# Kernel tuning notes

Measured on AMD Instinct MI355X. Metric: run time of the kernel, lower is better.

## Reference

```python
import jax, jax.numpy as jnp
import numpy as np

DROPOUT_P = 0.5  # eval-mode: hidden scaled by (1 - p) each step


def setup_inputs() -> dict:
    key = jax.random.key(0)
    ks = jax.random.split(key, 4)
    S, B, F, H = 512, 256, 256, 1024
    x = jax.random.normal(ks[0], (S, B, F), dtype=jnp.float32)
    W_i2h = jax.random.normal(ks[1], (H, F), dtype=jnp.float32) * 0.001
    b_i2h = jnp.zeros((H,), dtype=jnp.float32)
    W_h2h = jax.random.normal(ks[2], (H, H), dtype=jnp.float32) * 0.001
    init_hidden = jax.random.normal(ks[3], (1, 1, H), dtype=jnp.float32)
    return {"x": x, "W_i2h": W_i2h, "b_i2h": b_i2h, "W_h2h": W_h2h,
            "init_hidden": init_hidden, "batch_size": B}


def reference(x, W_i2h, b_i2h, W_h2h, init_hidden, batch_size):
    # x: [S, B, F] time-major. Output: final hidden [1, B, H].
    S, B, F = x.shape
    H = W_h2h.shape[0]
    keep = 1.0 - DROPOUT_P
    # Precompute input projections for all timesteps (batched GEMM).
    xi = jnp.einsum('sbf,hf->sbh', x, W_i2h) + b_i2h  # [S, B, H]
    # init_hidden [1,1,H] expanded to [B,H]
    h0 = jnp.broadcast_to(init_hidden[0], (B, H))

    def step(h, xi_t):
        # hidden = tanh(i2h(x_t) + h2h(keep * hidden))
        h_new = jnp.tanh(xi_t + (keep * h) @ W_h2h.T)
        return h_new, None

    h_final, _ = jax.lax.scan(step, h0, xi)
    return h_final[None]  # [1, B, H] matching torch broadcast shape
```

## Files before the change

kernel.cpp:

```cpp
#include <hip/hip_runtime.h>
#include <hip/hip_bf16.h>

#define S_LEN 512
#define B_SZ  256
#define F_SZ  256
#define H_SZ  1024
#define BH    (B_SZ * H_SZ)
#define KEEP  0.5f

typedef float f32x4 __attribute__((ext_vector_type(4)));
typedef short s16x8 __attribute__((ext_vector_type(8)));
typedef int   i32x4 __attribute__((ext_vector_type(4)));

static __device__ __forceinline__ short f2bf(float f) {
    unsigned u = __builtin_bit_cast(unsigned, f);
    unsigned r = u + 0x7fffu + ((u >> 16) & 1u);
    return (short)(r >> 16);
}

static __device__ __forceinline__ s16x8 pack8(f32x4 lo, f32x4 hi, float s) {
    s16x8 r;
#pragma unroll
    for (int i = 0; i < 4; ++i) { r[i] = f2bf(lo[i] * s); r[i + 4] = f2bf(hi[i] * s); }
    return r;
}

static __device__ __forceinline__ s16x8 pack8_pk(f32x4 lo, f32x4 hi) {
    int w0, w1, w2, w3;
    asm("v_cvt_pk_bf16_f32 %0, %1, %2" : "=v"(w0) : "v"(lo[0]), "v"(lo[1]));
    asm("v_cvt_pk_bf16_f32 %0, %1, %2" : "=v"(w1) : "v"(lo[2]), "v"(lo[3]));
    asm("v_cvt_pk_bf16_f32 %0, %1, %2" : "=v"(w2) : "v"(hi[0]), "v"(hi[1]));
    asm("v_cvt_pk_bf16_f32 %0, %1, %2" : "=v"(w3) : "v"(hi[2]), "v"(hi[3]));
    i32x4 r = { w0, w1, w2, w3 };
    return __builtin_bit_cast(s16x8, r);
}

static __device__ __forceinline__ long pack4_pk(f32x4 a) {
    int lo, hi;
    asm("v_cvt_pk_bf16_f32 %0, %1, %2" : "=v"(lo) : "v"(a[0]), "v"(a[1]));
    asm("v_cvt_pk_bf16_f32 %0, %1, %2" : "=v"(hi) : "v"(a[2]), "v"(a[3]));
    return (long)(((unsigned long)(unsigned)hi << 32) | (unsigned)lo);
}

static __device__ __forceinline__ f32x4 unpack4(long v) {
    unsigned lo = (unsigned)v, hi = (unsigned)((unsigned long)v >> 32);
    f32x4 r;
    r[0] = __builtin_bit_cast(float, lo << 16);
    r[1] = __builtin_bit_cast(float, lo & 0xffff0000u);
    r[2] = __builtin_bit_cast(float, hi << 16);
    r[3] = __builtin_bit_cast(float, hi & 0xffff0000u);
    return r;
}

static __device__ __forceinline__ float fast_tanh(float v) {
    float e = __expf(2.0f * v);
    return (e - 1.0f) / (e + 1.0f);
}

#define SYS_LD(p)   __hip_atomic_load((p), __ATOMIC_RELAXED, __HIP_MEMORY_SCOPE_SYSTEM)
#define SYS_ST(p,v) __hip_atomic_store((p), (v), __ATOMIC_RELAXED, __HIP_MEMORY_SCOPE_SYSTEM)
#define AGT_LD(p)   __hip_atomic_load((p), __ATOMIC_RELAXED, __HIP_MEMORY_SCOPE_AGENT)

template<int PURE>
static __device__ __forceinline__ int rmw_flag(int* p, int v) {
    int r;
    if constexpr (PURE)
        asm volatile("global_atomic_add %0, %1, %2, off sc0\n\ts_waitcnt vmcnt(0)"
                     : "=v"(r) : "v"(p), "v"(v) : "memory");
    else
        asm volatile("global_atomic_add %0, %1, %2, off sc0 sc1\n\ts_waitcnt vmcnt(0)"
                     : "=v"(r) : "v"(p), "v"(v) : "memory");
    return r;
}

template<int PURE>
static __device__ __forceinline__ void sig_flag(int* p) {
    int one = 1;
    if constexpr (PURE)
        asm volatile("global_atomic_add %0, %1, off" :: "v"(p), "v"(one) : "memory");
    else
        asm volatile("global_atomic_add %0, %1, off sc1" :: "v"(p), "v"(one) : "memory");
}

template<int PURE>
static __device__ __forceinline__ void sth(short* p, short v) {
    int vi = v;
    if constexpr (PURE)
        asm volatile("global_store_short %0, %1, off" :: "v"(p), "v"(vi) : "memory");
    else
        asm volatile("global_store_short %0, %1, off sc0 sc1" :: "v"(p), "v"(vi) : "memory");
}

#define MFMA(A, B, C) __builtin_amdgcn_mfma_f32_16x16x32_bf16((A), (B), (C), 0, 0, 0)

template<int PURE, int XI>
static __device__ __forceinline__ void step_loop(
    const float* __restrict__ x, const float* __restrict__ h0,
    float* __restrict__ out, short* __restrict__ hbuf, int* __restrict__ flags,
    const char* __restrict__ xi_lane, char* h_lds,
    const s16x8 (&wh)[32], const s16x8 (&wif)[8], float bj,
    int g, int b0, int role, int j, int wIdx, int wave, int lane, int tid, int dmask)
{
    const int ln = lane & 15;
    const int lk = lane >> 4;
    const int arow = b0 + ln;
    const int crow = b0 + lk * 4;
    const int xr = (ln & 7) << 4;
    const int rbase = ln * 2048 + lk * 16;
    int* const inbox  = flags + role * 64;
    int* const fanout = flags + ((g * 16 + lane) * 64 + wIdx);

    long xv = 0;
    if constexpr (XI) xv = *(const long*)xi_lane;

#pragma unroll 1
    for (int s = 0; s < S_LEN; ++s) {
        f32x4 acc[4];
        acc[1] = f32x4{ 0.f, 0.f, 0.f, 0.f };
        acc[2] = f32x4{ 0.f, 0.f, 0.f, 0.f };
        acc[3] = f32x4{ 0.f, 0.f, 0.f, 0.f };

        if constexpr (!XI) {
            acc[0] = f32x4{ bj, bj, bj, bj };
            const float* xp = x + ((size_t)s * B_SZ + arow) * F_SZ + lk * 8;
#pragma unroll
            for (int kf = 0; kf < 8; ++kf) {
                s16x8 a = pack8(*(const f32x4*)(xp + kf * 32),
                                *(const f32x4*)(xp + kf * 32 + 4), 1.0f);
                acc[kf & 1] = MFMA(a, wif[kf], acc[kf & 1]);
            }
        }

        if (s > 0) {
            if (wave == 0) {
                int it = 0;
                for (;;) {
                    int v = rmw_flag<PURE>(inbox + lane, 0);
                    if (__all(v >= s)) break;
                    if (++it > (1 << 14)) break;
                    __builtin_amdgcn_s_sleep(1);
                }
            }
            __syncthreads();

            const char* slice = (const char*)(hbuf + (size_t)((s - 1) & dmask) * BH
                                              + (size_t)b0 * H_SZ);
            long o[16];
#pragma unroll
            for (int r = 0; r < 16; ++r) {
                const long* p = (const long*)(slice + r * 2048) + tid;
                o[r] = PURE ? AGT_LD(p) : SYS_LD(p);
            }
#pragma unroll
            for (int r = 0; r < 16; ++r)
                *(long*)(h_lds + ((r * 2048 + tid * 8) ^ ((r & 7) << 4))) = o[r];
            __syncthreads();
            if constexpr (XI) acc[0] = unpack4(xv);

#pragma unroll
            for (int ks = 0; ks < 32; ++ks) {
                s16x8 a = *(const s16x8*)(h_lds + ((rbase + ks * 64) ^ xr));
                acc[ks & 3] = MFMA(a, wh[ks], acc[ks & 3]);
            }
        } else {
            if constexpr (XI) acc[0] = unpack4(xv);
#pragma unroll
            for (int ks = 0; ks < 32; ++ks) {
                const float* p = h0 + ks * 32 + lk * 8;
                s16x8 a = pack8(*(const f32x4*)p, *(const f32x4*)(p + 4), KEEP);
                acc[ks & 3] = MFMA(a, wh[ks], acc[ks & 3]);
            }
        }

        f32x4 r4 = (acc[0] + acc[1]) + (acc[2] + acc[3]);

        if (s < S_LEN - 1) {
            short* op = hbuf + (size_t)(s & dmask) * BH;
#pragma unroll
            for (int r = 0; r < 4; ++r)
                sth<PURE>(op + (crow + r) * H_SZ + j, f2bf(KEEP * fast_tanh(r4[r])));
            asm volatile("s_waitcnt vmcnt(0)" ::: "memory");
            if (lane < 16) sig_flag<PURE>(fanout);
            if constexpr (XI)
                xv = *(const long*)(xi_lane + (size_t)(s + 1) * (256u * 4 * 64 * 8));
        } else {
#pragma unroll
            for (int r = 0; r < 4; ++r)
                out[(crow + r) * H_SZ + j] = fast_tanh(r4[r]);
        }
    }
}

__global__ __launch_bounds__(256, 1) void xi_gemm(
    const float* __restrict__ x, const float* __restrict__ Wi,
    const float* __restrict__ bias, char* __restrict__ xi)
{
    const int bid  = blockIdx.x;
    const int role = bid & 255;
    const int c    = bid >> 8;
    const int g    = role >> 4;
    const int t    = role & 15;
    const int tid  = threadIdx.x;
    const int wave = tid >> 6;
    const int lane = tid & 63;
    const int ln   = lane & 15;
    const int lk   = lane >> 4;

    const int b0    = g * 16;
    const int jtile = t * 64;

    s16x8 wia[4][8];
    float b4[4];
#pragma unroll
    for (int jt = 0; jt < 4; ++jt) {
        b4[jt] = bias[jtile + jt * 16 + ln];
#pragma unroll
        for (int kf = 0; kf < 8; ++kf) {
            const float* p = Wi + (size_t)(jtile + jt * 16 + ln) * F_SZ
                           + kf * 32 + lk * 8;
            wia[jt][kf] = pack8_pk(*(const f32x4*)p, *(const f32x4*)(p + 4));
        }
    }

#pragma unroll 1
    for (int i = 0; i < 16; ++i) {
        const int s = c * 64 + wave + 4 * i;
        const float* xp = x + ((size_t)s * B_SZ + b0 + ln) * F_SZ + lk * 8;
        s16x8 af[8];
#pragma unroll
        for (int kf = 0; kf < 8; ++kf)
            af[kf] = pack8_pk(*(const f32x4*)(xp + kf * 32),
                              *(const f32x4*)(xp + kf * 32 + 4));
#pragma unroll
        for (int jt = 0; jt < 4; ++jt) {
            f32x4 a = { b4[jt], b4[jt], b4[jt], b4[jt] };
#pragma unroll
            for (int kf = 0; kf < 8; ++kf)
                a = MFMA(af[kf], wia[jt][kf], a);
            *(long*)(xi + ((((size_t)s * 256 + role) * 4 + jt) * 64 + lane) * 8)
                = pack4_pk(a);
        }
    }
}

template<int XI>
__global__ __launch_bounds__(256, 1) void rnn_fused(
    const float* __restrict__ x, const float* __restrict__ Wi,
    const float* __restrict__ bias, const float* __restrict__ Wh,
    const float* __restrict__ h0, float* __restrict__ out,
    short* __restrict__ hbuf, int* __restrict__ roster, int* __restrict__ flags,
    const char* __restrict__ xi, int dmask)
{
    __shared__ char h_lds[32768];
    __shared__ int sh_pure;
    const int bid  = blockIdx.x;
    const int role = ((bid & 7) << 5) | (bid >> 3);
    const int g    = role >> 4;
    const int t    = role & 15;
    const int tid  = threadIdx.x;
    const int wave = tid >> 6;
    const int lane = tid & 63;
    const int ln   = lane & 15;
    const int lk   = lane >> 4;

    int xcc;
    asm volatile("s_getreg_b32 %0, hwreg(HW_REG_XCC_ID)" : "=s"(xcc));
    xcc &= 7;

    if (tid == 0) SYS_ST(&roster[role], xcc + 1);
    if (tid < 16) {
        const int* rp = roster + g * 16 + tid;
        int v, it = 0;
        do { v = SYS_LD(rp); if (v) break; if (++it > (1 << 18)) break;
             __builtin_amdgcn_s_sleep(1); } while (1);
        int p = __all(v == __shfl(v, 0));
        if (tid == 0) sh_pure = p;
    }
    __syncthreads();
    const int pure = sh_pure;

    const int b0 = g * 16;
    const int j  = t * 64 + wave * 16 + ln;
    const int wIdx = t * 4 + wave;
    const char* xi_lane = xi + (((size_t)role * 4 + wave) * 64 + lane) * 8;

    s16x8 wh[32];
#pragma unroll
    for (int ks = 0; ks < 32; ++ks) {
        const float* p = Wh + (size_t)j * H_SZ + ks * 32 + lk * 8;
        wh[ks] = pack8(*(const f32x4*)p, *(const f32x4*)(p + 4), 1.0f);
    }
    s16x8 wif[8];
    if constexpr (!XI) {
#pragma unroll
        for (int kf = 0; kf < 8; ++kf) {
            const float* p = Wi + (size_t)j * F_SZ + kf * 32 + lk * 8;
            wif[kf] = pack8(*(const f32x4*)p, *(const f32x4*)(p + 4), 1.0f);
        }
    } else {
#pragma unroll
        for (int kf = 0; kf < 8; ++kf) wif[kf] = s16x8{0,0,0,0,0,0,0,0};
    }
    const float bj = XI ? 0.f : bias[j];

    if (pure)
        step_loop<1, XI>(x, h0, out, hbuf, flags, xi_lane, h_lds, wh, wif, bj,
                         g, b0, role, j, wIdx, wave, lane, tid, dmask);
    else
        step_loop<0, XI>(x, h0, out, hbuf, flags, xi_lane, h_lds, wh, wif, bj,
                         g, b0, role, j, wIdx, wave, lane, tid, dmask);
}

extern "C" void kernel_launch(void* const* d_in, const int* in_sizes, int n_in,
                              void* d_out, int out_size, void* d_ws, size_t ws_size,
                              hipStream_t stream) {
    const float* x  = (const float*)d_in[0];
    const float* Wi = (const float*)d_in[1];
    const float* bi = (const float*)d_in[2];
    const float* Wh = (const float*)d_in[3];
    const float* h0 = (const float*)d_in[4];
    float* out = (float*)d_out;

    int*   roster = (int*)d_ws;
    int*   flags  = (int*)((char*)d_ws + (4 << 10));
    short* hbuf   = (short*)((char*)d_ws + (128 << 10));
    char*  xi     = (char*)d_ws + (128 << 10) + 4 * (size_t)BH * 2;

    const size_t need4   = (128u << 10) + 4 * (size_t)BH * 2;
    const size_t need_xi = need4 + (size_t)S_LEN * 256 * 4 * 64 * 8;

    const int dmask = (ws_size >= need4) ? 3 : 1;

    (void)hipMemsetAsync(d_ws, 0, (68 << 10), stream);

    if (ws_size >= need_xi) {
        xi_gemm<<<dim3(2048), dim3(256), 0, stream>>>(x, Wi, bi, xi);
        rnn_fused<1><<<dim3(256), dim3(256), 0, stream>>>(
            x, Wi, bi, Wh, h0, out, hbuf, roster, flags, xi, dmask);
    } else {
        rnn_fused<0><<<dim3(256), dim3(256), 0, stream>>>(
            x, Wi, bi, Wh, h0, out, hbuf, roster, flags, nullptr, dmask);
    }
}
```

Measured before the change: 1.619 ms.

## Add fine-grained per-tile flag sync to overlap h gather with MFMA

Adds a step loop for the pure, precomputed-xi path in which each wave waits on per-producer-tile flags, copies that tile of the previous hidden state into swizzled LDS, and signals a local LDS flag. Consumers then start MFMAs on each group of four tiles as soon as they land, instead of waiting for the whole hidden slice. This is meant to overlap the cross-block synchronisation and global loads with the recurrent matmul. The cost is more flag polling traffic, spin loops with iteration caps that could silently proceed on timeout, and a slightly larger LDS allocation.

Result: slower. 6.162 ms (+280.6%).

```diff
diff --git a/kernel.cpp b/kernel.cpp
--- a/kernel.cpp
+++ b/kernel.cpp
@@ -191,6 +191,118 @@
     }
 }
 
+template<int XI>
+static __device__ __forceinline__ void step_loop_fine(
+    const float* __restrict__ h0, float* __restrict__ out,
+    short* __restrict__ hbuf, int* __restrict__ flags,
+    const char* __restrict__ xi_lane, char* h_lds,
+    const s16x8 (&wh)[32],
+    int g, int b0, int role, int t, int j, int wIdx, int wave, int lane, int tid,
+    int dmask)
+{
+    const int ln = lane & 15;
+    const int lk = lane >> 4;
+    const int crow = b0 + lk * 4;
+    volatile int* lflag = (volatile int*)(h_lds + 16 * 2048);
+    int* const inbox  = flags + role * 64;
+    int* const fanout = flags + ((g * 16 + lane) * 64 + wIdx);
+
+    const int srow = lane & 15;
+    const int su   = lane >> 4;
+
+    if (tid < 16) lflag[tid] = 0;
+    __syncthreads();
+
+    long xv = 0;
+    if constexpr (XI) xv = *(const long*)xi_lane;
+
+#pragma unroll 1
+    for (int s = 0; s < S_LEN; ++s) {
+        f32x4 acc[4];
+        acc[1] = f32x4{ 0.f, 0.f, 0.f, 0.f };
+        acc[2] = f32x4{ 0.f, 0.f, 0.f, 0.f };
+        acc[3] = f32x4{ 0.f, 0.f, 0.f, 0.f };
+
+        if (s > 0) {
+            const char* slice = (const char*)(hbuf + (size_t)((s - 1) & dmask) * BH
+                                              + (size_t)b0 * H_SZ);
+#pragma unroll 1
+            for (int i = 0; i < 4; ++i) {
+                const int tp = wave + i * 4;
+                int* sp = (lane < 4) ? (inbox + tp * 4 + lane)
+                                     : (inbox + t * 4 + (lane & 3));
+                int it = 0;
+                for (;;) {
+                    int v = (lane < 8) ? rmw_flag<1>(sp, 0) : s;
+                    if (__all(v >= s)) break;
+                    if (++it > (1 << 14)) break;
+                    __builtin_amdgcn_s_sleep(1);
+                }
+                const char* gb = slice + srow * 2048 + tp * 128;
+                char* lb = h_lds + tp * 2048 + srow * 128;
+                const int xw = (srow & 7) << 4;
+#pragma unroll
+                for (int q = 0; q < 4; ++q) {
+                    const int u = su + q * 4;
+                    long v = AGT_LD((const long*)(gb + u * 8));
+                    *(long*)(lb + ((u * 8) ^ xw)) = v;
+                }
+                __threadfence_block();
+                if (lane == 0) lflag[tp] = s;
+            }
+            if constexpr (XI) acc[0] = unpack4(xv);
+
+#pragma unroll 1
+            for (int c = 0; c < 4; ++c) {
+                int it = 0;
+                for (;;) {
+                    int v = (lane < 4) ? lflag[c * 4 + lane] : s;
+                    if (__all(v >= s)) break;
+                    if (++it > (1 << 16)) break;
+                }
+#pragma unroll
+                for (int t2 = 0; t2 < 4; ++t2) {
+                    const int tile = c * 4 + t2;
+                    const char* tb = h_lds + tile * 2048 + ln * 128;
+                    const int xr = (ln & 7) << 4;
+#pragma unroll
+                    for (int half = 0; half < 2; ++half) {
+                        const int ks = tile * 2 + half;
+                        s16x8 a = *(const s16x8*)(tb + ((half * 64 + lk * 16) ^ xr));
+                        acc[ks & 3] = MFMA(a, wh[ks], acc[ks & 3]);
+                    }
+                }
+            }
+        } else {
+            if constexpr (XI) acc[0] = unpack4(xv);
+            else acc[0] = f32x4{ 0.f, 0.f, 0.f, 0.f };
+#pragma unroll
+            for (int ks = 0; ks < 32; ++ks) {
+                const float* p = h0 + ks * 32 + lk * 8;
+                s16x8 a = pack8(*(const f32x4*)p, *(const f32x4*)(p + 4), KEEP);
+                acc[ks & 3] = MFMA(a, wh[ks], acc[ks & 3]);
+            }
+        }
+
+        f32x4 r4 = (acc[0] + acc[1]) + (acc[2] + acc[3]);
+
+        if (s < S_LEN - 1) {
+            short* op = hbuf + (size_t)(s & dmask) * BH;
+#pragma unroll
+            for (int r = 0; r < 4; ++r)
+                sth<1>(op + (crow + r) * H_SZ + j, f2bf(KEEP * fast_tanh(r4[r])));
+            asm volatile("s_waitcnt vmcnt(0)" ::: "memory");
+            if (lane < 16) sig_flag<1>(fanout);
+            if constexpr (XI)
+                xv = *(const long*)(xi_lane + (size_t)(s + 1) * (256u * 4 * 64 * 8));
+        } else {
+#pragma unroll
+            for (int r = 0; r < 4; ++r)
+                out[(crow + r) * H_SZ + j] = fast_tanh(r4[r]);
+        }
+    }
+}
+
 __global__ __launch_bounds__(256, 1) void xi_gemm(
     const float* __restrict__ x, const float* __restrict__ Wi,
     const float* __restrict__ bias, char* __restrict__ xi)
@@ -198,16 +310,14 @@
     const int bid  = blockIdx.x;
     const int role = bid & 255;
     const int c    = bid >> 8;
-    const int g    = role >> 4;
-    const int t    = role & 15;
     const int tid  = threadIdx.x;
     const int wave = tid >> 6;
     const int lane = tid & 63;
     const int ln   = lane & 15;
     const int lk   = lane >> 4;
 
-    const int b0    = g * 16;
-    const int jtile = t * 64;
+    const int b0    = (role >> 4) * 16;
+    const int jtile = (role & 15) * 64;
 
     s16x8 wia[4][8];
     float b4[4];
@@ -251,7 +361,7 @@
     short* __restrict__ hbuf, int* __restrict__ roster, int* __restrict__ flags,
     const char* __restrict__ xi, int dmask)
 {
-    __shared__ char h_lds[32768];
+    __shared__ char h_lds[32768 + 64];
     __shared__ int sh_pure;
     const int bid  = blockIdx.x;
     const int role = ((bid & 7) << 5) | (bid >> 3);
@@ -303,12 +413,16 @@
     }
     const float bj = XI ? 0.f : bias[j];
 
-    if (pure)
+    if (pure && XI) {
+        step_loop_fine<XI>(h0, out, hbuf, flags, xi_lane, h_lds, wh,
+                           g, b0, role, t, j, wIdx, wave, lane, tid, dmask);
+    } else if (pure) {
         step_loop<1, XI>(x, h0, out, hbuf, flags, xi_lane, h_lds, wh, wif, bj,
                          g, b0, role, j, wIdx, wave, lane, tid, dmask);
-    else
+    } else {
         step_loop<0, XI>(x, h0, out, hbuf, flags, xi_lane, h_lds, wh, wif, bj,
                          g, b0, role, j, wIdx, wave, lane, tid, dmask);
+    }
 }
 
 extern "C" void kernel_launch(void* const* d_in, const int* in_sizes, int n_in,
```

## Drop separate input-projection GEMM; fuse it into recurrent loop and overlap with flag wait

Applied to the files above, without the earlier changes.

Removes the standalone xi_gemm kernel and its bf16 workspace buffer. The recurrent kernel now computes the input projection itself each step. It prefetches the next step's raw x into registers right after signalling, and issues the x-projection MFMAs while the hidden-state loads are in flight. The goal is to hide the input projection inside the latency-bound recurrence instead of paying for a separate launch and the extra memory traffic. In exchange it adds 16 f32x4 registers and per-step packing work to the critical path of a kernel limited to one block per CU.

Measured after the change: 2.247 ms. 1.39x slower.

```diff
diff --git a/kernel.cpp b/kernel.cpp
--- a/kernel.cpp
+++ b/kernel.cpp
@@ -25,33 +25,6 @@
     return r;
 }
 
-static __device__ __forceinline__ s16x8 pack8_pk(f32x4 lo, f32x4 hi) {
-    int w0, w1, w2, w3;
-    asm("v_cvt_pk_bf16_f32 %0, %1, %2" : "=v"(w0) : "v"(lo[0]), "v"(lo[1]));
-    asm("v_cvt_pk_bf16_f32 %0, %1, %2" : "=v"(w1) : "v"(lo[2]), "v"(lo[3]));
-    asm("v_cvt_pk_bf16_f32 %0, %1, %2" : "=v"(w2) : "v"(hi[0]), "v"(hi[1]));
-    asm("v_cvt_pk_bf16_f32 %0, %1, %2" : "=v"(w3) : "v"(hi[2]), "v"(hi[3]));
-    i32x4 r = { w0, w1, w2, w3 };
-    return __builtin_bit_cast(s16x8, r);
-}
-
-static __device__ __forceinline__ long pack4_pk(f32x4 a) {
-    int lo, hi;
-    asm("v_cvt_pk_bf16_f32 %0, %1, %2" : "=v"(lo) : "v"(a[0]), "v"(a[1]));
-    asm("v_cvt_pk_bf16_f32 %0, %1, %2" : "=v"(hi) : "v"(a[2]), "v"(a[3]));
-    return (long)(((unsigned long)(unsigned)hi << 32) | (unsigned)lo);
-}
-
-static __device__ __forceinline__ f32x4 unpack4(long v) {
-    unsigned lo = (unsigned)v, hi = (unsigned)((unsigned long)v >> 32);
-    f32x4 r;
-    r[0] = __builtin_bit_cast(float, lo << 16);
-    r[1] = __builtin_bit_cast(float, lo & 0xffff0000u);
-    r[2] = __builtin_bit_cast(float, hi << 16);
-    r[3] = __builtin_bit_cast(float, hi & 0xffff0000u);
-    return r;
-}
-
 static __device__ __forceinline__ float fast_tanh(float v) {
     float e = __expf(2.0f * v);
     return (e - 1.0f) / (e + 1.0f);
@@ -93,12 +66,11 @@
 
 #define MFMA(A, B, C) __builtin_amdgcn_mfma_f32_16x16x32_bf16((A), (B), (C), 0, 0, 0)
 
-template<int PURE, int XI>
+template<int PURE>
 static __device__ __forceinline__ void step_loop(
     const float* __restrict__ x, const float* __restrict__ h0,
     float* __restrict__ out, short* __restrict__ hbuf, int* __restrict__ flags,
-    const char* __restrict__ xi_lane, char* h_lds,
-    const s16x8 (&wh)[32], const s16x8 (&wif)[8], float bj,
+    char* h_lds, const s16x8 (&wh)[32], const s16x8 (&wif)[8], float bj,
     int g, int b0, int role, int j, int wIdx, int wave, int lane, int tid, int dmask)
 {
     const int ln = lane & 15;
@@ -110,26 +82,23 @@
     int* const inbox  = flags + role * 64;
     int* const fanout = flags + ((g * 16 + lane) * 64 + wIdx);
 
-    long xv = 0;
-    if constexpr (XI) xv = *(const long*)xi_lane;
+    f32x4 xraw[16];
+    {
+        const float* xp = x + (size_t)arow * F_SZ + lk * 8;
+#pragma unroll
+        for (int kf = 0; kf < 8; ++kf) {
+            xraw[2 * kf]     = *(const f32x4*)(xp + kf * 32);
+            xraw[2 * kf + 1] = *(const f32x4*)(xp + kf * 32 + 4);
+        }
+    }
 
 #pragma unroll 1
     for (int s = 0; s < S_LEN; ++s) {
         f32x4 acc[4];
+        acc[0] = f32x4{ bj, bj, bj, bj };
         acc[1] = f32x4{ 0.f, 0.f, 0.f, 0.f };
         acc[2] = f32x4{ 0.f, 0.f, 0.f, 0.f };
         acc[3] = f32x4{ 0.f, 0.f, 0.f, 0.f };
-
-        if constexpr (!XI) {
-            acc[0] = f32x4{ bj, bj, bj, bj };
-            const float* xp = x + ((size_t)s * B_SZ + arow) * F_SZ + lk * 8;
-#pragma unroll
-            for (int kf = 0; kf < 8; ++kf) {
-                s16x8 a = pack8(*(const f32x4*)(xp + kf * 32),
-                                *(const f32x4*)(xp + kf * 32 + 4), 1.0f);
-                acc[kf & 1] = MFMA(a, wif[kf], acc[kf & 1]);
-            }
-        }
 
         if (s > 0) {
             if (wave == 0) {
@@ -151,11 +120,17 @@
                 const long* p = (const long*)(slice + r * 2048) + tid;
                 o[r] = PURE ? AGT_LD(p) : SYS_LD(p);
             }
+
+#pragma unroll
+            for (int kf = 0; kf < 8; ++kf) {
+                s16x8 a = pack8(xraw[2 * kf], xraw[2 * kf + 1], 1.0f);
+                acc[kf & 1] = MFMA(a, wif[kf], acc[kf & 1]);
+            }
+
 #pragma unroll
             for (int r = 0; r < 16; ++r)
                 *(long*)(h_lds + ((r * 2048 + tid * 8) ^ ((r & 7) << 4))) = o[r];
             __syncthreads();
-            if constexpr (XI) acc[0] = unpack4(xv);
 
 #pragma unroll
             for (int ks = 0; ks < 32; ++ks) {
@@ -163,7 +138,11 @@
                 acc[ks & 3] = MFMA(a, wh[ks], acc[ks & 3]);
             }
         } else {
-            if constexpr (XI) acc[0] = unpack4(xv);
+#pragma unroll
+            for (int kf = 0; kf < 8; ++kf) {
+                s16x8 a = pack8(xraw[2 * kf], xraw[2 * kf + 1], 1.0f);
+                acc[kf & 1] = MFMA(a, wif[kf], acc[kf & 1]);
+            }
 #pragma unroll
             for (int ks = 0; ks < 32; ++ks) {
                 const float* p = h0 + ks * 32 + lk * 8;
@@ -181,8 +160,13 @@
                 sth<PURE>(op + (crow + r) * H_SZ + j, f2bf(KEEP * fast_tanh(r4[r])));
             asm volatile("s_waitcnt vmcnt(0)" ::: "memory");
             if (lane < 16) sig_flag<PURE>(fanout);
-            if constexpr (XI)
-                xv = *(const long*)(xi_lane + (size_t)(s + 1) * (256u * 4 * 64 * 8));
+
+            const float* xp = x + ((size_t)(s + 1) * B_SZ + arow) * F_SZ + lk * 8;
+#pragma unroll
+            for (int kf = 0; kf < 8; ++kf) {
+                xraw[2 * kf]     = *(const f32x4*)(xp + kf * 32);
+                xraw[2 * kf + 1] = *(const f32x4*)(xp + kf * 32 + 4);
+            }
         } else {
 #pragma unroll
             for (int r = 0; r < 4; ++r)
@@ -191,65 +175,12 @@
     }
 }
 
-__global__ __launch_bounds__(256, 1) void xi_gemm(
-    const float* __restrict__ x, const float* __restrict__ Wi,
-    const float* __restrict__ bias, char* __restrict__ xi)
-{
-    const int bid  = blockIdx.x;
-    const int role = bid & 255;
-    const int c    = bid >> 8;
-    const int g    = role >> 4;
-    const int t    = role & 15;
-    const int tid  = threadIdx.x;
-    const int wave = tid >> 6;
-    const int lane = tid & 63;
-    const int ln   = lane & 15;
-    const int lk   = lane >> 4;
-
-    const int b0    = g * 16;
-    const int jtile = t * 64;
-
-    s16x8 wia[4][8];
-    float b4[4];
-#pragma unroll
-    for (int jt = 0; jt < 4; ++jt) {
-        b4[jt] = bias[jtile + jt * 16 + ln];
-#pragma unroll
-        for (int kf = 0; kf < 8; ++kf) {
-            const float* p = Wi + (size_t)(jtile + jt * 16 + ln) * F_SZ
-                           + kf * 32 + lk * 8;
-            wia[jt][kf] = pack8_pk(*(const f32x4*)p, *(const f32x4*)(p + 4));
-        }
-    }
-
-#pragma unroll 1
-    for (int i = 0; i < 16; ++i) {
-        const int s = c * 64 + wave + 4 * i;
-        const float* xp = x + ((size_t)s * B_SZ + b0 + ln) * F_SZ + lk * 8;
-        s16x8 af[8];
-#pragma unroll
-        for (int kf = 0; kf < 8; ++kf)
-            af[kf] = pack8_pk(*(const f32x4*)(xp + kf * 32),
-                              *(const f32x4*)(xp + kf * 32 + 4));
-#pragma unroll
-        for (int jt = 0; jt < 4; ++jt) {
-            f32x4 a = { b4[jt], b4[jt], b4[jt], b4[jt] };
-#pragma unroll
-            for (int kf = 0; kf < 8; ++kf)
-                a = MFMA(af[kf], wia[jt][kf], a);
-            *(long*)(xi + ((((size_t)s * 256 + role) * 4 + jt) * 64 + lane) * 8)
-                = pack4_pk(a);
-        }
-    }
-}
-
-template<int XI>
 __global__ __launch_bounds__(256, 1) void rnn_fused(
     const float* __restrict__ x, const float* __restrict__ Wi,
     const float* __restrict__ bias, const float* __restrict__ Wh,
     const float* __restrict__ h0, float* __restrict__ out,
     short* __restrict__ hbuf, int* __restrict__ roster, int* __restrict__ flags,
-    const char* __restrict__ xi, int dmask)
+    int dmask)
 {
     __shared__ char h_lds[32768];
     __shared__ int sh_pure;
@@ -282,7 +213,6 @@
     const int b0 = g * 16;
     const int j  = t * 64 + wave * 16 + ln;
     const int wIdx = t * 4 + wave;
-    const char* xi_lane = xi + (((size_t)role * 4 + wave) * 64 + lane) * 8;
 
     s16x8 wh[32];
 #pragma unroll
@@ -291,24 +221,19 @@
         wh[ks] = pack8(*(const f32x4*)p, *(const f32x4*)(p + 4), 1.0f);
     }
     s16x8 wif[8];
-    if constexpr (!XI) {
-#pragma unroll
-        for (int kf = 0; kf < 8; ++kf) {
-            const float* p = Wi + (size_t)j * F_SZ + kf * 32 + lk * 8;
-            wif[kf] = pack8(*(const f32x4*)p, *(const f32x4*)(p + 4), 1.0f);
-        }
-    } else {
-#pragma unroll
-        for (int kf = 0; kf < 8; ++kf) wif[kf] = s16x8{0,0,0,0,0,0,0,0};
-    }
-    const float bj = XI ? 0.f : bias[j];
+#pragma unroll
+    for (int kf = 0; kf < 8; ++kf) {
+        const float* p = Wi + (size_t)j * F_SZ + kf * 32 + lk * 8;
+        wif[kf] = pack8(*(const f32x4*)p, *(const f32x4*)(p + 4), 1.0f);
+    }
+    const float bj = bias[j];
 
     if (pure)
-        step_loop<1, XI>(x, h0, out, hbuf, flags, xi_lane, h_lds, wh, wif, bj,
-                         g, b0, role, j, wIdx, wave, lane, tid, dmask);
-    else
-        step_loop<0, XI>(x, h0, out, hbuf, flags, xi_lane, h_lds, wh, wif, bj,
-                         g, b0, role, j, wIdx, wave, lane, tid, dmask);
+        step_loop<1>(x, h0, out, hbuf, flags, h_lds, wh, wif, bj,
+                     g, b0, role, j, wIdx, wave, lane, tid, dmask);
+    else
+        step_loop<0>(x, h0, out, hbuf, flags, h_lds, wh, wif, bj,
+                     g, b0, role, j, wIdx, wave, lane, tid, dmask);
 }
 
 extern "C" void kernel_launch(void* const* d_in, const int* in_sizes, int n_in,
@@ -324,21 +249,12 @@
     int*   roster = (int*)d_ws;
     int*   flags  = (int*)((char*)d_ws + (4 << 10));
     short* hbuf   = (short*)((char*)d_ws + (128 << 10));
-    char*  xi     = (char*)d_ws + (128 << 10) + 4 * (size_t)BH * 2;
-
-    const size_t need4   = (128u << 10) + 4 * (size_t)BH * 2;
-    const size_t need_xi = need4 + (size_t)S_LEN * 256 * 4 * 64 * 8;
-
+
+    const size_t need4 = (128u << 10) + 4 * (size_t)BH * 2;
     const int dmask = (ws_size >= need4) ? 3 : 1;
 
     (void)hipMemsetAsync(d_ws, 0, (68 << 10), stream);
 
-    if (ws_size >= need_xi) {
-        xi_gemm<<<dim3(2048), dim3(256), 0, stream>>>(x, Wi, bi, xi);
-        rnn_fused<1><<<dim3(256), dim3(256), 0, stream>>>(
-            x, Wi, bi, Wh, h0, out, hbuf, roster, flags, xi, dmask);
-    } else {
-        rnn_fused<0><<<dim3(256), dim3(256), 0, stream>>>(
-            x, Wi, bi, Wh, h0, out, hbuf, roster, flags, nullptr, dmask);
-    }
-}
+    rnn_fused<<<dim3(256), dim3(256), 0, stream>>>(
+        x, Wi, bi, Wh, h0, out, hbuf, roster, flags, dmask);
+}
```
